# Kernel optimization log

Hardware: AMD Instinct MI355X
Metric: run time of the kernel (lower is better)

## Reference

```python
import jax, jax.numpy as jnp
import numpy as np

N_NODES = 200000
N_EDGES = 6400000


def setup_inputs() -> dict:
    key = jax.random.key(0)
    ks = jax.random.split(key, 6)
    x = jax.random.normal(ks[0], (N_NODES, 11), dtype=jnp.float32)
    edge_index = jax.random.randint(ks[1], (2, N_EDGES), 0, N_NODES, dtype=jnp.int64)
    # orthogonal-ish init approximated by scaled gaussian; math path is identical
    W1 = jax.random.normal(ks[2], (11, 11), dtype=jnp.float32) / jnp.sqrt(11.0)
    W2 = jax.random.normal(ks[3], (11, 11), dtype=jnp.float32) / jnp.sqrt(11.0)
    W3 = jax.random.normal(ks[4], (11, 16), dtype=jnp.float32) / jnp.sqrt(11.0)
    b1 = jnp.zeros((11,), jnp.float32)
    b2 = jnp.zeros((11,), jnp.float32)
    b3 = jnp.zeros((16,), jnp.float32)
    return {"x": x, "edge_index": edge_index, "W1": W1, "b1": b1,
            "W2": W2, "b2": b2, "W3": W3, "b3": b3}


def gcn_conv(x, W, b, src, dst, n):
    """PyG GCNConv with add_self_loops=True, symmetric normalization.
    out_i = sum_{j->i} d_j^{-1/2} d_i^{-1/2} (x_j W) + d_i^{-1} (x_i W) + b
    where d includes the self-loop (+1).
    """
    h = x @ W                                                  # [N, F_out]
    deg = jax.ops.segment_sum(jnp.ones(src.shape[0], h.dtype), dst,
                              num_segments=n) + 1.0            # self-loop
    dinv = jax.lax.rsqrt(deg)                                  # [N]
    norm = dinv[src] * dinv[dst]                               # [E]
    agg = jax.ops.segment_sum(norm[:, None] * h[src], dst, num_segments=n)
    agg = agg + (dinv * dinv)[:, None] * h                     # self-loop term
    return agg + b


def reference(x, edge_index, W1, b1, W2, b2, W3, b3):
    n = x.shape[0]
    src, dst = edge_index[0], edge_index[1]
    h = jax.nn.relu(gcn_conv(x, W1, b1, src, dst, n))   # dropout p=0.0 -> identity
    h = jax.nn.relu(gcn_conv(h, W2, b2, src, dst, n))
    return gcn_conv(h, W3, b3, src, dst, n)
```

## Files before the change

### kernel.cpp

```cpp
#include <hip/hip_runtime.h>

#define N_NODES 200000
#define N_EDGES 6400000

constexpr int BSHIFT = 9;
constexpr int NBUCK  = (N_NODES + 511) / 512;
constexpr int CHUNK  = 16384;
constexpr int NCHUNK = (N_EDGES + CHUNK - 1) / CHUNK;
constexpr int MAXBUCK = 18432;
constexpr int SEGSTRIDE = 2052;
constexpr int SEGMAX = 1536;

__device__ __forceinline__ int ld_edge(const void* ei, int is64, int idx) {
    return is64 ? (int)((const long long*)ei)[idx] : ((const int*)ei)[idx];
}

__global__ void k_zero(int* __restrict__ p, int n) {
    int i = blockIdx.x * blockDim.x + threadIdx.x;
    if (i < n) p[i] = 0;
}

__global__ void k_iota(int* __restrict__ cursor) {
    int i = threadIdx.x;
    if (i < NBUCK) cursor[i] = i * MAXBUCK;
}

__global__ void k_detect(const unsigned int* __restrict__ ei, int* __restrict__ flag) {
    __shared__ int nz;
    if (threadIdx.x == 0) nz = 0;
    __syncthreads();
    if (ei[2 * threadIdx.x + 1] != 0u) atomicOr(&nz, 1);
    __syncthreads();
    if (threadIdx.x == 0) *flag = nz ? 0 : 1;
}

__global__ void __launch_bounds__(1024)
k_binscatter(const void* __restrict__ ei, const int* __restrict__ flag,
             int* __restrict__ bucketCursor, unsigned int* __restrict__ bin) {
    __shared__ int hist[NBUCK];
    __shared__ int pref[NBUCK + 1];
    __shared__ int cur[NBUCK];
    __shared__ int gb[NBUCK];
    __shared__ int sc[512];
    __shared__ unsigned int stage[CHUNK];
    const int is64 = *flag;
    int b = blockIdx.x, t = threadIdx.x;
    int e0 = b * CHUNK;
    int n = min(CHUNK, N_EDGES - e0);
    for (int i = t; i < NBUCK; i += 1024) hist[i] = 0;
    __syncthreads();
    for (int i = t; i < n; i += 1024) {
        int d = ld_edge(ei, is64, N_EDGES + e0 + i);
        atomicAdd(&hist[d >> BSHIFT], 1);
    }
    __syncthreads();
    if (t < 256) {
        sc[t]       = (t < NBUCK)       ? hist[t]       : 0;
        sc[t + 256] = (t + 256 < NBUCK) ? hist[t + 256] : 0;
    }
    __syncthreads();
    for (int off = 1; off < 512; off <<= 1) {
        int a0 = 0, a1 = 0;
        if (t < 256) {
            a0 = (t >= off) ? sc[t - off] : 0;
            a1 = sc[t + 256 - off];
        }
        __syncthreads();
        if (t < 256) { sc[t] += a0; sc[t + 256] += a1; }
        __syncthreads();
    }
    for (int i = t; i < NBUCK; i += 1024) {
        int excl = sc[i] - hist[i];
        pref[i] = excl;
        cur[i] = excl;
    }
    if (t == 0) pref[NBUCK] = n;
    __syncthreads();
    for (int i = t; i < n; i += 1024) {
        int s = ld_edge(ei, is64, e0 + i);
        int d = ld_edge(ei, is64, N_EDGES + e0 + i);
        int bk = d >> BSHIFT;
        unsigned int q = (unsigned int)s / 50000u;
        int p = atomicAdd(&cur[bk], 1);
        stage[p] = (q << 27) | ((unsigned int)(d & 511) << 18) | (unsigned int)s;
    }
    __syncthreads();
    for (int i = t; i < NBUCK; i += 1024) {
        int c = hist[i];
        gb[i] = c ? atomicAdd(&bucketCursor[i], c) : 0;
    }
    __syncthreads();
    int wave = t >> 6, lane = t & 63;
    for (int i = wave; i < NBUCK; i += 16) {
        int c = hist[i];
        if (!c) continue;
        int gg = gb[i];
        int room = (i + 1) * MAXBUCK - gg;
        int lim = min(c, max(room, 0));
        int pp = pref[i];
        for (int j = lane; j < lim; j += 64) bin[gg + j] = stage[pp + j];
    }
}

__global__ void __launch_bounds__(1024)
k_bucketsort(const int* __restrict__ bucketCursor, unsigned int* __restrict__ bin,
             float* __restrict__ dinv, unsigned short* __restrict__ seg16) {
    __shared__ int cnt[2048];
    __shared__ int cur[2048];
    __shared__ int tsum[1024];
    __shared__ unsigned int payload[MAXBUCK];
    int b = blockIdx.x, t = threadIdx.x;
    int base = b * MAXBUCK;
    int n = min(bucketCursor[b] - base, MAXBUCK);
    cnt[t] = 0; cnt[t + 1024] = 0;
    __syncthreads();
    for (int i = t; i < n; i += 1024) {
        unsigned int u = bin[base + i];
        int key = (int)((u >> 27) << 9) | (int)((u >> 18) & 511u);
        atomicAdd(&cnt[key], 1);
    }
    __syncthreads();
    int b0 = t * 2;
    int s = cnt[b0] + cnt[b0 + 1];
    tsum[t] = s;
    __syncthreads();
    int v = s;
    for (int off = 1; off < 1024; off <<= 1) {
        int add = (t >= off) ? tsum[t - off] : 0;
        __syncthreads();
        tsum[t] += add;
        __syncthreads();
    }
    int run = tsum[t] - v;
    cur[b0] = run;
    cur[b0 + 1] = run + cnt[b0];
    __syncthreads();
    for (int i = t; i < 2048; i += 1024)
        seg16[b * SEGSTRIDE + i] = (unsigned short)cur[i];
    if (t == 0) seg16[b * SEGSTRIDE + 2048] = (unsigned short)n;
    int node0 = b << BSHIFT;
    if (t < 512) {
        int node = node0 + t;
        if (node < N_NODES) {
            int deg = cnt[t] + cnt[512 + t] + cnt[1024 + t] + cnt[1536 + t];
            dinv[node] = rsqrtf((float)deg + 1.0f);
        }
    }
    __syncthreads();
    for (int i = t; i < n; i += 1024) {
        unsigned int u = bin[base + i];
        int key = (int)((u >> 27) << 9) | (int)((u >> 18) & 511u);
        int p = atomicAdd(&cur[key], 1);
        if (p < MAXBUCK) payload[p] = (u & 0x3FFFFu) << 4;
    }
    __syncthreads();
    for (int i = t; i < n; i += 1024) bin[base + i] = payload[i];
}

template <int FIN, int FOUT, int SIN>
__global__ void k_xw(const float* xin, const float* __restrict__ W,
                     const float* __restrict__ dinv, float* hs) {
    __shared__ float sW[FIN * FOUT];
    int t = threadIdx.x;
    if (t < FIN * FOUT) sW[t] = W[t];
    __syncthreads();
    int i = blockIdx.x * 256 + t;
    if (i >= N_NODES) return;
    float xi[FIN];
#pragma unroll
    for (int k = 0; k < FIN; ++k) xi[k] = xin[i * SIN + k];
    float di = dinv[i];
    float o[FOUT];
#pragma unroll
    for (int j = 0; j < FOUT; ++j) {
        float acc = 0.f;
#pragma unroll
        for (int k = 0; k < FIN; ++k) acc += xi[k] * sW[k * FOUT + j];
        o[j] = di * acc;
    }
#pragma unroll
    for (int j = 0; j < FOUT; ++j) hs[i * 16 + j] = o[j];
}

template <int FIN, int FOUT>
__global__ void k_fx(float* __restrict__ B, float* __restrict__ accG,
                     const float* __restrict__ dinv,
                     const float* __restrict__ biasPrev,
                     const float* __restrict__ Wnext) {
    __shared__ float sW[FIN * FOUT];
    __shared__ float sb[FIN];
    int t = threadIdx.x;
    if (t < FIN * FOUT) sW[t] = Wnext[t];
    if (t < FIN) sb[t] = biasPrev[t];
    __syncthreads();
    int i = blockIdx.x * 256 + t;
    if (i >= N_NODES) return;
    float di = dinv[i];
    float xi[FIN];
#pragma unroll
    for (int k = 0; k < FIN; ++k) {
        float v = di * (accG[i * 16 + k] + B[i * 16 + k]) + sb[k];
        xi[k] = fmaxf(v, 0.f);
    }
#pragma unroll
    for (int c = 0; c < 16; ++c) accG[i * 16 + c] = 0.f;
    float o[FOUT];
#pragma unroll
    for (int j = 0; j < FOUT; ++j) {
        float acc = 0.f;
#pragma unroll
        for (int k = 0; k < FIN; ++k) acc += xi[k] * sW[k * FOUT + j];
        o[j] = di * acc;
    }
#pragma unroll
    for (int j = 0; j < FOUT; ++j) B[i * 16 + j] = o[j];
}

__global__ void __launch_bounds__(512)
k_agg(const unsigned short* __restrict__ seg16,
      const unsigned int* __restrict__ bin, const float* __restrict__ hs,
      float* __restrict__ accG) {
    __shared__ unsigned short s_sr[132];
    __shared__ unsigned int s_bin[SEGMAX];
    int blk = blockIdx.x;
    int q = blk & 3;
    int Q = (blk >> 2) & 3;
    int b = blk >> 4;
    int t = threadIdx.x;
    int base = b * MAXBUCK;
    const unsigned short* sr = seg16 + b * SEGSTRIDE + (q << 9) + (Q << 7);
    if (t < 129) s_sr[t] = sr[t];
    __syncthreads();
    int s0 = (int)s_sr[0];
    int nseg = (int)s_sr[128] - s0;
    bool staged = (nseg <= SEGMAX);
    if (staged) {
        for (int i = t; i < nseg; i += 512) s_bin[i] = bin[base + s0 + i];
    }
    __syncthreads();
    int g = t >> 4, f = t & 15;
    int dd0 = g << 2;
    int r0 = (int)s_sr[dd0 + 0], r1 = (int)s_sr[dd0 + 1], r2 = (int)s_sr[dd0 + 2];
    int r3 = (int)s_sr[dd0 + 3], r4 = (int)s_sr[dd0 + 4];
    int n0 = r1 - r0, n1 = r2 - r1, n2 = r3 - r2, n3 = r4 - r3;
    float a0 = 0.f, a1 = 0.f, a2 = 0.f, a3 = 0.f;
    int m = max(max(n0, n1), max(n2, n3));
    if (staged) {
        int o0 = r0 - s0, o1 = r1 - s0, o2 = r2 - s0, o3 = r3 - s0;
#pragma unroll 2
        for (int k = 0; k < m; k += 2) {
            float t00 = 0.f, t01 = 0.f, t10 = 0.f, t11 = 0.f;
            float t20 = 0.f, t21 = 0.f, t30 = 0.f, t31 = 0.f;
            if (k     < n0) t00 = hs[s_bin[o0 + k]     + f];
            if (k + 1 < n0) t01 = hs[s_bin[o0 + k + 1] + f];
            if (k     < n1) t10 = hs[s_bin[o1 + k]     + f];
            if (k + 1 < n1) t11 = hs[s_bin[o1 + k + 1] + f];
            if (k     < n2) t20 = hs[s_bin[o2 + k]     + f];
            if (k + 1 < n2) t21 = hs[s_bin[o2 + k + 1] + f];
            if (k     < n3) t30 = hs[s_bin[o3 + k]     + f];
            if (k + 1 < n3) t31 = hs[s_bin[o3 + k + 1] + f];
            a0 += t00 + t01;
            a1 += t10 + t11;
            a2 += t20 + t21;
            a3 += t30 + t31;
        }
    } else {
        const unsigned int* p0 = bin + base + r0;
        const unsigned int* p1 = bin + base + r1;
        const unsigned int* p2 = bin + base + r2;
        const unsigned int* p3 = bin + base + r3;
#pragma unroll 2
        for (int k = 0; k < m; ++k) {
            if (k < n0) a0 += hs[p0[k] + f];
            if (k < n1) a1 += hs[p1[k] + f];
            if (k < n2) a2 += hs[p2[k] + f];
            if (k < n3) a3 += hs[p3[k] + f];
        }
    }
    int node0 = (b << BSHIFT) + (Q << 7) + dd0;
    if (node0 + 0 < N_NODES) unsafeAtomicAdd(&accG[((node0 + 0) << 4) + f], a0);
    if (node0 + 1 < N_NODES) unsafeAtomicAdd(&accG[((node0 + 1) << 4) + f], a1);
    if (node0 + 2 < N_NODES) unsafeAtomicAdd(&accG[((node0 + 2) << 4) + f], a2);
    if (node0 + 3 < N_NODES) unsafeAtomicAdd(&accG[((node0 + 3) << 4) + f], a3);
}

template <int F, bool RELU>
__global__ void k_finish(float* __restrict__ B, float* __restrict__ accG,
                         const float* __restrict__ dinv,
                         const float* __restrict__ bias, float* __restrict__ out) {
    int i = blockIdx.x * blockDim.x + threadIdx.x;
    if (i >= N_NODES * 16) return;
    int node = i >> 4, ff = i & 15;
    float di = dinv[node];
    if (ff < F) {
        float r = di * (accG[i] + B[i]) + bias[ff];
        if (RELU) r = fmaxf(r, 0.f);
        out[node * 16 + ff] = r;
    }
}

extern "C" void kernel_launch(void* const* d_in, const int* in_sizes, int n_in,
                              void* d_out, int out_size, void* d_ws, size_t ws_size,
                              hipStream_t stream) {
    const float* x  = (const float*)d_in[0];
    const void*  ei = d_in[1];
    const float* W1 = (const float*)d_in[2];
    const float* b1 = (const float*)d_in[3];
    const float* W2 = (const float*)d_in[4];
    const float* b2 = (const float*)d_in[5];
    const float* W3 = (const float*)d_in[6];
    const float* b3 = (const float*)d_in[7];
    float* out = (float*)d_out;

    char* w = (char*)d_ws;
    int*   bucketCursor = (int*)(w + 0);
    int*   flag         = (int*)(w + 2048);
    float* dinv         = (float*)(w + 2112);
    unsigned short* seg16 = (unsigned short*)(w + 802112);
    unsigned int* bin   = (unsigned int*)(w + 2406784);
    float* B            = (float*)(w + 31234432);
    float* accG         = out;

    k_zero<<<12500, 256, 0, stream>>>((int*)accG, N_NODES * 16);
    k_iota<<<1, 512, 0, stream>>>(bucketCursor);
    k_detect<<<1, 256, 0, stream>>>((const unsigned int*)ei, flag);
    k_binscatter<<<NCHUNK, 1024, 0, stream>>>(ei, flag, bucketCursor, bin);
    k_bucketsort<<<NBUCK, 1024, 0, stream>>>(bucketCursor, bin, dinv, seg16);

    k_xw<11, 11, 11><<<782, 256, 0, stream>>>(x, W1, dinv, B);
    k_agg<<<NBUCK * 16, 512, 0, stream>>>(seg16, bin, B, accG);
    k_fx<11, 11><<<782, 256, 0, stream>>>(B, accG, dinv, b1, W2);
    k_agg<<<NBUCK * 16, 512, 0, stream>>>(seg16, bin, B, accG);
    k_fx<11, 16><<<782, 256, 0, stream>>>(B, accG, dinv, b2, W3);
    k_agg<<<NBUCK * 16, 512, 0, stream>>>(seg16, bin, B, accG);
    k_finish<16, false><<<12500, 256, 0, stream>>>(B, accG, dinv, b3, out);
}
```

Baseline: 293.6 us.

## Vectorize aggregation gathers to float4 and widen blocks to whole buckets

The aggregation kernel now gathers each neighbor's 16-float feature row with four float4 loads, one per lane, instead of sixteen scalar loads. Each block covers a full 512-node bucket slice rather than a quarter of it, so the grid has a quarter as many blocks. The larger staging buffer allows up to 6144 edge indices per block in LDS. Results are written through an LDS tile and then flushed with coalesced atomics. This cuts load-instruction count and per-block overhead, at the cost of fewer blocks, more LDS per block and longer serial per-thread loops on skewed degrees.

Result: slower. 323.1 us (+10.1%).

```diff
diff --git a/kernel.cpp b/kernel.cpp
--- a/kernel.cpp
+++ b/kernel.cpp
@@ -9,7 +9,9 @@
 constexpr int NCHUNK = (N_EDGES + CHUNK - 1) / CHUNK;
 constexpr int MAXBUCK = 18432;
 constexpr int SEGSTRIDE = 2052;
-constexpr int SEGMAX = 1536;
+constexpr int SEGMAX2 = 6144;
+
+typedef float v4f __attribute__((ext_vector_type(4)));
 
 __device__ __forceinline__ int ld_edge(const void* ei, int is64, int idx) {
     return is64 ? (int)((const long long*)ei)[idx] : ((const int*)ei)[idx];
@@ -220,45 +222,50 @@
 k_agg(const unsigned short* __restrict__ seg16,
       const unsigned int* __restrict__ bin, const float* __restrict__ hs,
       float* __restrict__ accG) {
-    __shared__ unsigned short s_sr[132];
-    __shared__ unsigned int s_bin[SEGMAX];
+    __shared__ unsigned short s_sr[520];
+    __shared__ unsigned int s_mem[8192];
     int blk = blockIdx.x;
     int q = blk & 3;
-    int Q = (blk >> 2) & 3;
-    int b = blk >> 4;
+    int b = blk >> 2;
     int t = threadIdx.x;
     int base = b * MAXBUCK;
-    const unsigned short* sr = seg16 + b * SEGSTRIDE + (q << 9) + (Q << 7);
-    if (t < 129) s_sr[t] = sr[t];
+    const unsigned short* sr = seg16 + b * SEGSTRIDE + (q << 9);
+    s_sr[t] = sr[t];
+    if (t == 0) s_sr[512] = sr[512];
     __syncthreads();
     int s0 = (int)s_sr[0];
-    int nseg = (int)s_sr[128] - s0;
-    bool staged = (nseg <= SEGMAX);
+    int nseg = (int)s_sr[512] - s0;
+    unsigned int* s_bin = s_mem;
+    bool staged = (nseg <= SEGMAX2);
     if (staged) {
         for (int i = t; i < nseg; i += 512) s_bin[i] = bin[base + s0 + i];
     }
     __syncthreads();
-    int g = t >> 4, f = t & 15;
+    int g = t >> 2, l = t & 3;
     int dd0 = g << 2;
+    const v4f* hs4 = (const v4f*)hs;
     int r0 = (int)s_sr[dd0 + 0], r1 = (int)s_sr[dd0 + 1], r2 = (int)s_sr[dd0 + 2];
     int r3 = (int)s_sr[dd0 + 3], r4 = (int)s_sr[dd0 + 4];
     int n0 = r1 - r0, n1 = r2 - r1, n2 = r3 - r2, n3 = r4 - r3;
-    float a0 = 0.f, a1 = 0.f, a2 = 0.f, a3 = 0.f;
+    v4f a0 = {0.f,0.f,0.f,0.f}, a1 = {0.f,0.f,0.f,0.f};
+    v4f a2 = {0.f,0.f,0.f,0.f}, a3 = {0.f,0.f,0.f,0.f};
     int m = max(max(n0, n1), max(n2, n3));
     if (staged) {
         int o0 = r0 - s0, o1 = r1 - s0, o2 = r2 - s0, o3 = r3 - s0;
 #pragma unroll 2
         for (int k = 0; k < m; k += 2) {
-            float t00 = 0.f, t01 = 0.f, t10 = 0.f, t11 = 0.f;
-            float t20 = 0.f, t21 = 0.f, t30 = 0.f, t31 = 0.f;
-            if (k     < n0) t00 = hs[s_bin[o0 + k]     + f];
-            if (k + 1 < n0) t01 = hs[s_bin[o0 + k + 1] + f];
-            if (k     < n1) t10 = hs[s_bin[o1 + k]     + f];
-            if (k + 1 < n1) t11 = hs[s_bin[o1 + k + 1] + f];
-            if (k     < n2) t20 = hs[s_bin[o2 + k]     + f];
-            if (k + 1 < n2) t21 = hs[s_bin[o2 + k + 1] + f];
-            if (k     < n3) t30 = hs[s_bin[o3 + k]     + f];
-            if (k + 1 < n3) t31 = hs[s_bin[o3 + k + 1] + f];
+            v4f t00 = {0.f,0.f,0.f,0.f}, t01 = {0.f,0.f,0.f,0.f};
+            v4f t10 = {0.f,0.f,0.f,0.f}, t11 = {0.f,0.f,0.f,0.f};
+            v4f t20 = {0.f,0.f,0.f,0.f}, t21 = {0.f,0.f,0.f,0.f};
+            v4f t30 = {0.f,0.f,0.f,0.f}, t31 = {0.f,0.f,0.f,0.f};
+            if (k     < n0) t00 = hs4[(s_bin[o0 + k]     >> 2) + l];
+            if (k + 1 < n0) t01 = hs4[(s_bin[o0 + k + 1] >> 2) + l];
+            if (k     < n1) t10 = hs4[(s_bin[o1 + k]     >> 2) + l];
+            if (k + 1 < n1) t11 = hs4[(s_bin[o1 + k + 1] >> 2) + l];
+            if (k     < n2) t20 = hs4[(s_bin[o2 + k]     >> 2) + l];
+            if (k + 1 < n2) t21 = hs4[(s_bin[o2 + k + 1] >> 2) + l];
+            if (k     < n3) t30 = hs4[(s_bin[o3 + k]     >> 2) + l];
+            if (k + 1 < n3) t31 = hs4[(s_bin[o3 + k + 1] >> 2) + l];
             a0 += t00 + t01;
             a1 += t10 + t11;
             a2 += t20 + t21;
@@ -271,17 +278,27 @@
         const unsigned int* p3 = bin + base + r3;
 #pragma unroll 2
         for (int k = 0; k < m; ++k) {
-            if (k < n0) a0 += hs[p0[k] + f];
-            if (k < n1) a1 += hs[p1[k] + f];
-            if (k < n2) a2 += hs[p2[k] + f];
-            if (k < n3) a3 += hs[p3[k] + f];
+            if (k < n0) a0 += hs4[(p0[k] >> 2) + l];
+            if (k < n1) a1 += hs4[(p1[k] >> 2) + l];
+            if (k < n2) a2 += hs4[(p2[k] >> 2) + l];
+            if (k < n3) a3 += hs4[(p3[k] >> 2) + l];
         }
     }
-    int node0 = (b << BSHIFT) + (Q << 7) + dd0;
-    if (node0 + 0 < N_NODES) unsafeAtomicAdd(&accG[((node0 + 0) << 4) + f], a0);
-    if (node0 + 1 < N_NODES) unsafeAtomicAdd(&accG[((node0 + 1) << 4) + f], a1);
-    if (node0 + 2 < N_NODES) unsafeAtomicAdd(&accG[((node0 + 2) << 4) + f], a2);
-    if (node0 + 3 < N_NODES) unsafeAtomicAdd(&accG[((node0 + 3) << 4) + f], a3);
+    __syncthreads();
+    float* accL = (float*)s_mem;
+    int lc = l << 2;
+    *(v4f*)&accL[(dd0 + 0) * 16 + lc] = a0;
+    *(v4f*)&accL[(dd0 + 1) * 16 + lc] = a1;
+    *(v4f*)&accL[(dd0 + 2) * 16 + lc] = a2;
+    *(v4f*)&accL[(dd0 + 3) * 16 + lc] = a3;
+    __syncthreads();
+    int node0 = b << BSHIFT;
+#pragma unroll
+    for (int i = t; i < 8192; i += 512) {
+        int node = node0 + (i >> 4);
+        if (node < N_NODES)
+            unsafeAtomicAdd(&accG[(node << 4) + (i & 15)], accL[i]);
+    }
 }
 
 template <int F, bool RELU>
@@ -328,10 +345,10 @@
     k_bucketsort<<<NBUCK, 1024, 0, stream>>>(bucketCursor, bin, dinv, seg16);
 
     k_xw<11, 11, 11><<<782, 256, 0, stream>>>(x, W1, dinv, B);
-    k_agg<<<NBUCK * 16, 512, 0, stream>>>(seg16, bin, B, accG);
+    k_agg<<<NBUCK * 4, 512, 0, stream>>>(seg16, bin, B, accG);
     k_fx<11, 11><<<782, 256, 0, stream>>>(B, accG, dinv, b1, W2);
-    k_agg<<<NBUCK * 16, 512, 0, stream>>>(seg16, bin, B, accG);
+    k_agg<<<NBUCK * 4, 512, 0, stream>>>(seg16, bin, B, accG);
     k_fx<11, 16><<<782, 256, 0, stream>>>(B, accG, dinv, b2, W3);
-    k_agg<<<NBUCK * 16, 512, 0, stream>>>(seg16, bin, B, accG);
+    k_agg<<<NBUCK * 4, 512, 0, stream>>>(seg16, bin, B, accG);
     k_finish<16, false><<<12500, 256, 0, stream>>>(B, accG, dinv, b3, out);
 }
```
